# Optimization experiments

Hardware: AMD Instinct MI355X
Metric: run time of the kernel (lower is better)

## Reference

```python
import jax, jax.numpy as jnp
import numpy as np

KERNEL_SIGMA2 = 4096.0  # = 2 * x_dim, assumed Gaussian RBF kernel

B, K, D, H, Z = 512, 32, 2048, 512, 64


def setup_inputs() -> dict:
    key = jax.random.key(0)
    ks = jax.random.split(key, 8)
    s = lambda k, shp, fan: jax.random.normal(k, shp, jnp.float32) / np.sqrt(fan)
    return {
        "x_c": jax.random.normal(ks[0], (B, D), jnp.float32),
        "x_nn": jax.random.normal(ks[1], (B, K, D), jnp.float32),
        "W1": s(ks[2], (D, H), D), "b1": jnp.zeros((H,), jnp.float32),
        "W2": s(ks[3], (H, Z), H), "b2": jnp.zeros((Z,), jnp.float32),
        "V1": s(ks[4], (Z, H), Z), "c1": jnp.zeros((H,), jnp.float32),
        "V2": s(ks[5], (H, D), H), "c2": jnp.zeros((D,), jnp.float32),
    }


def _enc(x, W1, b1, W2, b2):
    return jax.nn.relu(x @ W1 + b1) @ W2 + b2


def _dec(z, V1, c1, V2, c2):
    return jax.nn.relu(z @ V1 + c1) @ V2 + c2


def reference(x_c, x_nn, W1, b1, W2, b2, V1, c1, V2, c2):
    bs, num_nn, x_dim = x_nn.shape
    z_c = _enc(x_c, W1, b1, W2, b2)                       # [B, Z]
    z_dim = z_c.shape[1]
    z_nn = _enc(x_nn.reshape(bs * num_nn, x_dim), W1, b1, W2, b2)
    z_nn = z_nn.reshape(bs, num_nn, z_dim)
    dz = z_nn - z_c[:, None, :]                           # [B, K, Z]

    # first-order Taylor: recon(z_c) + J(z_c) @ dz via JVP of decoder
    dec_fn = lambda z: _dec(z, V1, c1, V2, c2)
    inputs = jnp.broadcast_to(z_c[:, None, :], (bs, num_nn, z_dim)).reshape(-1, z_dim)
    _, Jdz = jax.jvp(dec_fn, (inputs,), (dz.reshape(-1, z_dim),))  # [B*K, D]

    recon = dec_fn(z_c)                                   # [B, D]
    n_recon = recon[:, None, :] + Jdz.reshape(bs, num_nn, x_dim)

    diff = x_nn - n_recon
    n_loss = jnp.sum(diff * diff, axis=2)                 # ||.||^2, [B, K]
    w = jnp.exp(-jnp.sum((x_nn - x_c[:, None, :]) ** 2, axis=2) / KERNEL_SIGMA2)
    return jnp.mean(w * n_loss)
```

## Files before the change

kernel.cpp:

```cpp
#include <hip/hip_runtime.h>
#include <hip/hip_bf16.h>
#include <cstdint>
#include <cstddef>

#define DEV __device__ __forceinline__

typedef __bf16 bf16;
typedef __bf16 bf16x8 __attribute__((ext_vector_type(8)));
typedef float f32x4 __attribute__((ext_vector_type(4)));

DEV f32x4 mfma16(bf16x8 a, bf16x8 b, f32x4 c) {
  return __builtin_amdgcn_mfma_f32_16x16x32_bf16(a, b, c, 0, 0, 0);
}

DEV void glds16(const void* g, void* l) {
  __builtin_amdgcn_global_load_lds(
      (const __attribute__((address_space(1))) void*)g,
      (__attribute__((address_space(3))) void*)l, 16, 0, 0);
}

template<int ROWS, int NT>
DEV void stage_tile(const bf16* __restrict__ src, int ld, int row0, int k0,
                    unsigned char* lds, int tid) {
  constexpr int CALLS = (ROWS * 128) / (NT * 16);
  const int wid = tid >> 6, lane = tid & 63;
#pragma unroll
  for (int c = 0; c < CALLS; ++c) {
    const int obase = c * (NT * 16) + wid * 1024;
    const int o = obase + lane * 16;
    const int row = o >> 7;
    const int scb = (o & 127) ^ ((row & 7) << 4);
    glds16(src + (size_t)(row0 + row) * ld + k0 + (scb >> 1), lds + obase);
  }
}

template<int BM, int BN, int WM, int WN, int MODE, int CASTR, int MINW = 2>
__global__ __launch_bounds__(WM*WN*64, MINW) void gemm_kernel(
    const bf16* __restrict__ A, const float* __restrict__ Af,
    const float* __restrict__ Af2,
    const bf16* __restrict__ Bt, const float* __restrict__ bias,
    int M, int N, int K,
    float* __restrict__ out32, bf16* __restrict__ out16,
    const float* __restrict__ hc, const float* __restrict__ recon,
    float* __restrict__ nloss, float* __restrict__ warg)
{
  constexpr int NT = WM * WN * 64;
  constexpr int FM = (BM / WM) / 16;
  constexpr int FN = (BN / WN) / 16;
  constexpr int HALF = (BM + BN) * 128;
  __shared__ __align__(16) unsigned char smem[CASTR ? 2 * HALF : HALF];

  const int tid = threadIdx.x, lane = tid & 63, wid = tid >> 6;
  const int wm = wid / WN, wn = wid % WN;
  const int wm0 = wm * (BM / WM), wn0 = wn * (BN / WN);

  int bx = blockIdx.x, by = blockIdx.y;
  {
    const int gx = gridDim.x;
    const int nwg = gx * gridDim.y;
    if ((nwg & 7) == 0) {
      const int fid = by * gx + bx;
      const int cpx = nwg >> 3;
      const int w = (fid & 7) * cpx + (fid >> 3);
      bx = w % gx; by = w / gx;
    }
  }
  const int i0 = by * BM, j0 = bx * BN;
  const int l15 = lane & 15, lg = lane >> 4;

  f32x4 acc[FM][FN] = {};

  int arow[FM], brow[FN];
#pragma unroll
  for (int mi = 0; mi < FM; ++mi) arow[mi] = wm0 + mi * 16 + l15;
#pragma unroll
  for (int ni = 0; ni < FN; ++ni) brow[ni] = wn0 + ni * 16 + l15;

  auto compute = [&](const unsigned char* cA, const unsigned char* cB) {
#pragma unroll
    for (int kh = 0; kh < 2; ++kh) {
      const int koff = kh * 64 + lg * 16;
      bf16x8 af[FM], bfr[FN];
#pragma unroll
      for (int mi = 0; mi < FM; ++mi) {
        const int off = (arow[mi] * 128 + koff) ^ ((arow[mi] & 7) << 4);
        af[mi] = *reinterpret_cast<const bf16x8*>(cA + off);
      }
#pragma unroll
      for (int ni = 0; ni < FN; ++ni) {
        const int off = (brow[ni] * 128 + koff) ^ ((brow[ni] & 7) << 4);
        bfr[ni] = *reinterpret_cast<const bf16x8*>(cB + off);
      }
#pragma unroll
      for (int mi = 0; mi < FM; ++mi)
#pragma unroll
        for (int ni = 0; ni < FN; ++ni)
          acc[mi][ni] = mfma16(af[mi], bfr[ni], acc[mi][ni]);
    }
  };

  if constexpr (CASTR) {
    constexpr int QCH = (BM * 8) / NT;
    const float* As = (i0 < 512) ? Af + (size_t)i0 * K
                                 : Af2 + (size_t)(i0 - 512) * K;
    float4 areg[2 * QCH];

    auto loadA = [&](int kt) {
#pragma unroll
      for (int j = 0; j < QCH; ++j) {
        const int q = j * NT + tid;
        const int row = q >> 3, c8 = q & 7;
        const float* p = As + (size_t)row * K + kt + c8 * 8;
        areg[2 * j]     = *(const float4*)p;
        areg[2 * j + 1] = *(const float4*)(p + 4);
      }
    };
    auto writeA = [&](unsigned char* dA) {
#pragma unroll
      for (int j = 0; j < QCH; ++j) {
        const int q = j * NT + tid;
        const int row = q >> 3, c8 = q & 7;
        bf16x8 v;
        v[0] = (bf16)areg[2*j].x;   v[1] = (bf16)areg[2*j].y;
        v[2] = (bf16)areg[2*j].z;   v[3] = (bf16)areg[2*j].w;
        v[4] = (bf16)areg[2*j+1].x; v[5] = (bf16)areg[2*j+1].y;
        v[6] = (bf16)areg[2*j+1].z; v[7] = (bf16)areg[2*j+1].w;
        *(bf16x8*)(dA + ((row * 128 + c8 * 16) ^ ((row & 7) << 4))) = v;
      }
    };

    unsigned char* cur = smem;
    unsigned char* nxt = smem + HALF;
    const int NTIL = K >> 6;
    loadA(0);
    stage_tile<BN, NT>(Bt, K, j0, 0, cur + BM * 128, tid);
    for (int t = 0; t < NTIL; ++t) {
      __syncthreads();
      writeA(cur);
      __syncthreads();
      if (t + 1 < NTIL) {
        loadA((t + 1) << 6);
        stage_tile<BN, NT>(Bt, K, j0, (t + 1) << 6, nxt + BM * 128, tid);
        __builtin_amdgcn_sched_barrier(0);
      }
      compute(cur, cur + BM * 128);
      unsigned char* sw = cur; cur = nxt; nxt = sw;
    }
  } else {
    for (int kt = 0; kt < K; kt += 64) {
      stage_tile<BM, NT>(A, K, i0, kt, smem, tid);
      stage_tile<BN, NT>(Bt, K, j0, kt, smem + BM * 128, tid);
      __syncthreads();
      compute(smem, smem + BM * 128);
      __syncthreads();
    }
  }

  if constexpr (MODE == 5) {
    float* eb = (float*)smem;
#pragma unroll
    for (int mi = 0; mi < FM; ++mi) {
      __syncthreads();
#pragma unroll
      for (int ni = 0; ni < FN; ++ni) {
        const int col = wn0 + ni * 16 + l15;
        const int lr0 = wm * 16 + lg * 4;
#pragma unroll
        for (int r = 0; r < 4; ++r)
          eb[(lr0 + r) * 132 + col] = acc[mi][ni][r];
      }
      __syncthreads();
      const int lrow = tid >> 3;
      const int c0 = (tid & 7) * 16;
      const int grow = i0 + (lrow >> 4) * 64 + mi * 16 + (lrow & 15);
      const int b = grow >> 5;
      const float* xp = Af2  + (size_t)grow * 2048 + j0 + c0;
      const float* cp = Af   + (size_t)b * 2048 + j0 + c0;
      const float* rp = recon + (size_t)b * 2048 + j0 + c0;
      float nl = 0.f, wa = 0.f;
#pragma unroll
      for (int q4 = 0; q4 < 4; ++q4) {
        const float4 xv = *(const float4*)(xp + q4 * 4);
        const float4 cv = *(const float4*)(cp + q4 * 4);
        const float4 rv = *(const float4*)(rp + q4 * 4);
#pragma unroll
        for (int q = 0; q < 4; ++q) {
          const float xf = ((const float*)&xv)[q];
          const float d = xf - ((const float*)&rv)[q] - eb[lrow * 132 + c0 + q4 * 4 + q];
          nl += d * d;
          const float wd = xf - ((const float*)&cv)[q];
          wa += wd * wd;
        }
      }
      nl += __shfl_xor(nl, 1, 64); wa += __shfl_xor(wa, 1, 64);
      nl += __shfl_xor(nl, 2, 64); wa += __shfl_xor(wa, 2, 64);
      nl += __shfl_xor(nl, 4, 64); wa += __shfl_xor(wa, 4, 64);
      if ((tid & 7) == 0) {
        atomicAdd(&nloss[grow], nl);
        atomicAdd(&warg[grow], wa);
      }
    }
  } else {
#pragma unroll
    for (int mi = 0; mi < FM; ++mi) {
#pragma unroll
      for (int ni = 0; ni < FN; ++ni) {
#pragma unroll
        for (int r = 0; r < 4; ++r) {
          const int row = i0 + wm0 + mi * 16 + lg * 4 + r;
          const int col = j0 + wn0 + ni * 16 + l15;
          float v = acc[mi][ni][r];
          if constexpr (MODE == 0) {
            v += bias[col];
            out16[(size_t)row * N + col] = (bf16)fmaxf(v, 0.f);
          } else if constexpr (MODE == 1) {
            v += bias[col];
            out32[(size_t)row * N + col] = v;
          } else if constexpr (MODE == 2) {
            v += bias[col];
            out32[(size_t)row * N + col] = v;
            out16[(size_t)row * N + col] = (bf16)fmaxf(v, 0.f);
          } else if constexpr (MODE == 4) {
            const int b = row >> 5;
            const float m = hc[(size_t)b * 512 + col];
            out16[(size_t)row * N + col] = (bf16)(m > 0.f ? v : 0.f);
          }
        }
      }
    }
  }
}

__global__ void transpose_all_kernel(
    const float* __restrict__ W1, const float* __restrict__ W2,
    const float* __restrict__ V1, const float* __restrict__ V2,
    bf16* __restrict__ W1t, bf16* __restrict__ W2t,
    bf16* __restrict__ V1t, bf16* __restrict__ V2t) {
  int blk = blockIdx.x;
  const float* src; bf16* dst; int R, C, gx;
  if (blk < 1024)      { src = W1; dst = W1t; R = 2048; C = 512;  gx = 16; }
  else if (blk < 1056) { blk -= 1024; src = W2; dst = W2t; R = 512; C = 64;   gx = 2;  }
  else if (blk < 1088) { blk -= 1056; src = V1; dst = V1t; R = 64;  C = 512;  gx = 16; }
  else                 { blk -= 1088; src = V2; dst = V2t; R = 512; C = 2048; gx = 64; }
  __shared__ float t[32][33];
  const int c0 = (blk % gx) * 32, r0 = (blk / gx) * 32;
  const int tx = threadIdx.x, ty = threadIdx.y;
#pragma unroll
  for (int i = 0; i < 32; i += 8)
    t[ty + i][tx] = src[(size_t)(r0 + ty + i) * C + c0 + tx];
  __syncthreads();
#pragma unroll
  for (int i = 0; i < 32; i += 8)
    dst[(size_t)(c0 + ty + i) * R + r0 + tx] = (bf16)t[tx][ty + i];
}

__global__ void dz_prep_kernel(const float* __restrict__ z,
                               bf16* __restrict__ dzb,
                               bf16* __restrict__ zcb,
                               float* __restrict__ nw,
                               float* __restrict__ out) {
  const int i = blockIdx.x * 256 + threadIdx.x;
  if (i < 32768) nw[i] = 0.f;
  if (i == 0) out[0] = 0.f;
  const int r = i >> 6, j = i & 63;
  const float v = z[i];
  if (r < 512) {
    zcb[i] = (bf16)v;
  } else {
    const int rn = r - 512;
    const int b = rn >> 5;
    dzb[(size_t)rn * 64 + j] = (bf16)(v - z[(size_t)b * 64 + j]);
  }
}

__global__ void finalize_kernel(const float* __restrict__ nloss,
                                const float* __restrict__ warg,
                                float* __restrict__ out) {
  const int i = blockIdx.x * 256 + threadIdx.x;
  float v = expf(-warg[i] * (1.0f / 4096.0f)) * nloss[i] * (1.0f / 16384.0f);
#pragma unroll
  for (int s = 1; s < 64; s <<= 1) v += __shfl_xor(v, s, 64);
  __shared__ float red[4];
  const int lane = threadIdx.x & 63, w = threadIdx.x >> 6;
  if (lane == 0) red[w] = v;
  __syncthreads();
  if (threadIdx.x == 0) atomicAdd(out, red[0] + red[1] + red[2] + red[3]);
}

extern "C" void kernel_launch(void* const* d_in, const int* in_sizes, int n_in,
                              void* d_out, int out_size, void* d_ws, size_t ws_size,
                              hipStream_t stream) {
  const float* x_c = (const float*)d_in[0];
  const float* x_nn = (const float*)d_in[1];
  const float* W1 = (const float*)d_in[2];
  const float* b1 = (const float*)d_in[3];
  const float* W2 = (const float*)d_in[4];
  const float* b2 = (const float*)d_in[5];
  const float* V1 = (const float*)d_in[6];
  const float* c1 = (const float*)d_in[7];
  const float* V2 = (const float*)d_in[8];
  const float* c2 = (const float*)d_in[9];
  float* out = (float*)d_out;
  char* ws = (char*)d_ws;

  size_t off = 0;
  auto take = [&](size_t n) { size_t o = off; off += n; return o; };
  bf16*  W1t   = (bf16*) (ws + take((size_t)512 * 2048 * 2));
  bf16*  W2t   = (bf16*) (ws + take((size_t)64 * 512 * 2));
  bf16*  V1t   = (bf16*) (ws + take((size_t)512 * 64 * 2));
  bf16*  V2t   = (bf16*) (ws + take((size_t)2048 * 512 * 2));
  bf16*  h1    = (bf16*) (ws + take((size_t)16896 * 512 * 2));
  float* z     = (float*)(ws + take((size_t)16896 * 64 * 4));
  bf16*  dzb   = (bf16*) (ws + take((size_t)16384 * 64 * 2));
  bf16*  zcb   = (bf16*) (ws + take((size_t)512 * 64 * 2));
  float* hc    = (float*)(ws + take((size_t)512 * 512 * 4));
  bf16*  acb   = (bf16*) (ws + take((size_t)512 * 512 * 2));
  float* recon = (float*)(ws + take((size_t)512 * 2048 * 4));
  bf16*  dab   = (bf16*) (ws + take((size_t)16384 * 512 * 2));
  float* nloss = (float*)(ws + take((size_t)16384 * 4));
  float* warg  = (float*)(ws + take((size_t)16384 * 4));

  transpose_all_kernel<<<dim3(2112), dim3(32, 8), 0, stream>>>(
      W1, W2, V1, V2, W1t, W2t, V1t, V2t);

  gemm_kernel<64, 256, 1, 4, 0, 1, 2><<<dim3(2, 264), dim3(256), 0, stream>>>(
      nullptr, x_c, x_nn, W1t, b1, 16896, 512, 2048,
      nullptr, h1, nullptr, nullptr, nullptr, nullptr);

  gemm_kernel<64, 64, 2, 2, 1, 0><<<dim3(1, 264), dim3(256), 0, stream>>>(
      h1, nullptr, nullptr, W2t, b2, 16896, 64, 512,
      z, nullptr, nullptr, nullptr, nullptr, nullptr);

  dz_prep_kernel<<<dim3(4224), dim3(256), 0, stream>>>(z, dzb, zcb, nloss, out);

  gemm_kernel<128, 128, 2, 2, 2, 0><<<dim3(4, 4), dim3(256), 0, stream>>>(
      zcb, nullptr, nullptr, V1t, c1, 512, 512, 64,
      hc, acb, nullptr, nullptr, nullptr, nullptr);

  gemm_kernel<64, 128, 2, 2, 1, 0><<<dim3(16, 8), dim3(256), 0, stream>>>(
      acb, nullptr, nullptr, V2t, c2, 512, 2048, 512,
      recon, nullptr, nullptr, nullptr, nullptr, nullptr);

  gemm_kernel<128, 128, 2, 2, 4, 0><<<dim3(4, 128), dim3(256), 0, stream>>>(
      dzb, nullptr, nullptr, V1t, nullptr, 16384, 512, 64,
      nullptr, dab, hc, nullptr, nullptr, nullptr);

  gemm_kernel<128, 128, 2, 2, 5, 0><<<dim3(16, 128), dim3(256), 0, stream>>>(
      dab, x_c, x_nn, V2t, nullptr, 16384, 2048, 512,
      nullptr, nullptr, nullptr, recon, nloss, warg);

  finalize_kernel<<<dim3(64), dim3(256), 0, stream>>>(nloss, warg, out);
}
```

Baseline: 183.9 us.

## Stage fp32 A tiles directly to LDS and convert to bf16 at fragment load

The first encoder GEMM no longer loads fp32 activations into registers and writes converted bf16 into double-buffered LDS. It now DMAs raw fp32 tiles straight into LDS with global_load_lds and converts to bf16 when reading MFMA fragments. The tile shape also changes from 64x256 with 1x4 warps to 64x128 with 2x2 warps, doubling the grid. This removes register staging and VGPR pressure, but gives up double buffering. It also doubles LDS traffic for A, and each wave repeats the conversion.

```diff
diff --git a/kernel.cpp b/kernel.cpp
--- a/kernel.cpp
+++ b/kernel.cpp
@@ -34,7 +34,22 @@
   }
 }
 
-template<int BM, int BN, int WM, int WN, int MODE, int CASTR, int MINW = 2>
+template<int ROWS, int NT>
+DEV void stage_tile_f32(const float* __restrict__ src, int ld, int row0, int k0,
+                        unsigned char* lds, int tid) {
+  constexpr int CALLS = (ROWS * 256) / (NT * 16);
+  const int wid = tid >> 6, lane = tid & 63;
+#pragma unroll
+  for (int c = 0; c < CALLS; ++c) {
+    const int obase = c * (NT * 16) + wid * 1024;
+    const int o = obase + lane * 16;
+    const int row = o >> 8;
+    const int scb = (o & 255) ^ ((row & 7) << 4);
+    glds16(src + (size_t)(row0 + row) * ld + k0 + (scb >> 2), lds + obase);
+  }
+}
+
+template<int BM, int BN, int WM, int WN, int MODE, int AF32, int MINW = 2>
 __global__ __launch_bounds__(WM*WN*64, MINW) void gemm_kernel(
     const bf16* __restrict__ A, const float* __restrict__ Af,
     const float* __restrict__ Af2,
@@ -48,7 +63,7 @@
   constexpr int FM = (BM / WM) / 16;
   constexpr int FN = (BN / WN) / 16;
   constexpr int HALF = (BM + BN) * 128;
-  __shared__ __align__(16) unsigned char smem[CASTR ? 2 * HALF : HALF];
+  __shared__ __align__(16) unsigned char smem[AF32 ? (BM * 256 + BN * 128) : HALF];
 
   const int tid = threadIdx.x, lane = tid & 63, wid = tid >> 6;
   const int wm = wid / WN, wn = wid % WN;
@@ -79,16 +94,32 @@
   auto compute = [&](const unsigned char* cA, const unsigned char* cB) {
 #pragma unroll
     for (int kh = 0; kh < 2; ++kh) {
-      const int koff = kh * 64 + lg * 16;
       bf16x8 af[FM], bfr[FN];
-#pragma unroll
-      for (int mi = 0; mi < FM; ++mi) {
-        const int off = (arow[mi] * 128 + koff) ^ ((arow[mi] & 7) << 4);
-        af[mi] = *reinterpret_cast<const bf16x8*>(cA + off);
-      }
+      if constexpr (AF32) {
+        const int Fb = kh * 128 + lg * 32;
+#pragma unroll
+        for (int mi = 0; mi < FM; ++mi) {
+          const int r = arow[mi];
+          const unsigned char* p = cA + r * 256;
+          const f32x4 lo = *reinterpret_cast<const f32x4*>(p + ((Fb)      ^ ((r & 7) << 4)));
+          const f32x4 hi = *reinterpret_cast<const f32x4*>(p + ((Fb + 16) ^ ((r & 7) << 4)));
+          bf16x8 a;
+          a[0] = (bf16)lo[0]; a[1] = (bf16)lo[1]; a[2] = (bf16)lo[2]; a[3] = (bf16)lo[3];
+          a[4] = (bf16)hi[0]; a[5] = (bf16)hi[1]; a[6] = (bf16)hi[2]; a[7] = (bf16)hi[3];
+          af[mi] = a;
+        }
+      } else {
+        const int koff = kh * 64 + lg * 16;
+#pragma unroll
+        for (int mi = 0; mi < FM; ++mi) {
+          const int off = (arow[mi] * 128 + koff) ^ ((arow[mi] & 7) << 4);
+          af[mi] = *reinterpret_cast<const bf16x8*>(cA + off);
+        }
+      }
+      const int koffB = kh * 64 + lg * 16;
 #pragma unroll
       for (int ni = 0; ni < FN; ++ni) {
-        const int off = (brow[ni] * 128 + koff) ^ ((brow[ni] & 7) << 4);
+        const int off = (brow[ni] * 128 + koffB) ^ ((brow[ni] & 7) << 4);
         bfr[ni] = *reinterpret_cast<const bf16x8*>(cB + off);
       }
 #pragma unroll
@@ -99,52 +130,15 @@
     }
   };
 
-  if constexpr (CASTR) {
-    constexpr int QCH = (BM * 8) / NT;
+  if constexpr (AF32) {
     const float* As = (i0 < 512) ? Af + (size_t)i0 * K
                                  : Af2 + (size_t)(i0 - 512) * K;
-    float4 areg[2 * QCH];
-
-    auto loadA = [&](int kt) {
-#pragma unroll
-      for (int j = 0; j < QCH; ++j) {
-        const int q = j * NT + tid;
-        const int row = q >> 3, c8 = q & 7;
-        const float* p = As + (size_t)row * K + kt + c8 * 8;
-        areg[2 * j]     = *(const float4*)p;
-        areg[2 * j + 1] = *(const float4*)(p + 4);
-      }
-    };
-    auto writeA = [&](unsigned char* dA) {
-#pragma unroll
-      for (int j = 0; j < QCH; ++j) {
-        const int q = j * NT + tid;
-        const int row = q >> 3, c8 = q & 7;
-        bf16x8 v;
-        v[0] = (bf16)areg[2*j].x;   v[1] = (bf16)areg[2*j].y;
-        v[2] = (bf16)areg[2*j].z;   v[3] = (bf16)areg[2*j].w;
-        v[4] = (bf16)areg[2*j+1].x; v[5] = (bf16)areg[2*j+1].y;
-        v[6] = (bf16)areg[2*j+1].z; v[7] = (bf16)areg[2*j+1].w;
-        *(bf16x8*)(dA + ((row * 128 + c8 * 16) ^ ((row & 7) << 4))) = v;
-      }
-    };
-
-    unsigned char* cur = smem;
-    unsigned char* nxt = smem + HALF;
-    const int NTIL = K >> 6;
-    loadA(0);
-    stage_tile<BN, NT>(Bt, K, j0, 0, cur + BM * 128, tid);
-    for (int t = 0; t < NTIL; ++t) {
-      __syncthreads();
-      writeA(cur);
-      __syncthreads();
-      if (t + 1 < NTIL) {
-        loadA((t + 1) << 6);
-        stage_tile<BN, NT>(Bt, K, j0, (t + 1) << 6, nxt + BM * 128, tid);
-        __builtin_amdgcn_sched_barrier(0);
-      }
-      compute(cur, cur + BM * 128);
-      unsigned char* sw = cur; cur = nxt; nxt = sw;
+    for (int kt = 0; kt < K; kt += 64) {
+      stage_tile_f32<BM, NT>(As, K, 0, kt, smem, tid);
+      stage_tile<BN, NT>(Bt, K, j0, kt, smem + BM * 256, tid);
+      __syncthreads();
+      compute(smem, smem + BM * 256);
+      __syncthreads();
     }
   } else {
     for (int kt = 0; kt < K; kt += 64) {
@@ -323,7 +317,7 @@
   transpose_all_kernel<<<dim3(2112), dim3(32, 8), 0, stream>>>(
       W1, W2, V1, V2, W1t, W2t, V1t, V2t);
 
-  gemm_kernel<64, 256, 1, 4, 0, 1, 2><<<dim3(2, 264), dim3(256), 0, stream>>>(
+  gemm_kernel<64, 128, 2, 2, 0, 1><<<dim3(4, 264), dim3(256), 0, stream>>>(
       nullptr, x_c, x_nn, W1t, b1, 16896, 512, 2048,
       nullptr, h1, nullptr, nullptr, nullptr, nullptr);
 
```

Result: faster. 168.6 us (-8.3%).
